# Kernel tuning notes

Hardware: AMD Instinct MI355X
Metric: run time of the kernel (lower is better)

## Reference

```python
import jax, jax.numpy as jnp
import numpy as np

N = 10000; E = 60000; D = 3000; H = 512; L = 128; P = 256
NUM_MASK = 3000  # int(0.3 * N)

def prelu(x, a):
    return jnp.where(x >= 0, x, a * x)

def setup_inputs() -> dict:
    key = jax.random.key(0)
    ks = jax.random.split(key, 32)
    def rn(k, shape, scale=0.02):
        return jax.random.normal(k, shape, jnp.float32) * scale
    inp = {
        'x': jax.random.normal(ks[0], (N, D), jnp.float32),
        'edge_index': jax.random.randint(ks[1], (2, E), 0, N),
        'perm': jax.random.permutation(ks[2], N),
        'shuffle': jax.random.permutation(ks[3], N - NUM_MASK),
        's_W1': rn(ks[4], (D, H)), 's_b1': jnp.zeros((H,), jnp.float32), 's_a': jnp.full((1,), 0.25, jnp.float32),
        's_W2': rn(ks[5], (H, L)), 's_b2': jnp.zeros((L,), jnp.float32),
        't_W1': rn(ks[6], (D, H)), 't_b1': jnp.zeros((H,), jnp.float32), 't_a': jnp.full((1,), 0.25, jnp.float32),
        't_W2': rn(ks[7], (H, L)), 't_b2': jnp.zeros((L,), jnp.float32),
        'p_W1': rn(ks[8], (L, P)), 'p_b1': jnp.zeros((P,), jnp.float32), 'p_a': jnp.full((1,), 0.25, jnp.float32),
        'p_W2': rn(ks[9], (P, L)), 'p_b2': jnp.zeros((L,), jnp.float32),
        'tp_W1': rn(ks[10], (L, P)), 'tp_b1': jnp.zeros((P,), jnp.float32), 'tp_a': jnp.full((1,), 0.25, jnp.float32),
        'tp_W2': rn(ks[11], (P, L)), 'tp_b2': jnp.zeros((L,), jnp.float32),
        'dgi_W': rn(ks[12], (L, L), 0.05),
        'pos_token': rn(ks[13], (1, D)), 'neg_token': rn(ks[14], (1, D)),
        'e2d_W': rn(ks[15], (L, L), 0.05),
        'd_W': rn(ks[16], (L, D)), 'd_b': jnp.zeros((D,), jnp.float32),
    }
    return inp

def reference(x, edge_index, perm, shuffle, s_W1, s_b1, s_a, s_W2, s_b2, t_W1, t_b1, t_a, t_W2, t_b2, p_W1, p_b1, p_a, p_W2, p_b2, tp_W1, tp_b1, tp_a, tp_W2, tp_b2, dgi_W, pos_token, neg_token, e2d_W, d_W, d_b):
    n = x.shape[0]
    # GCN normalization with added self loops (PyG gcn_norm, flow source->target)
    loops = jnp.arange(n)
    src = jnp.concatenate([edge_index[0], loops])
    dst = jnp.concatenate([edge_index[1], loops])
    deg = jax.ops.segment_sum(jnp.ones(dst.shape, x.dtype), dst, n)
    dinv = jnp.where(deg > 0, jax.lax.rsqrt(deg), 0.0)
    enorm = (dinv[src] * dinv[dst])[:, None]  # [E+N, 1]

    def gcn(h, W, b):
        h = h @ W  # transform first, then propagate (PyG GCNConv)
        return jax.ops.segment_sum(h[src] * enorm, dst, n) + b

    # feature masking / corruption (bn=False -> Identity; no dropout at eval)
    mask_nodes = perm[:NUM_MASK]
    keep_nodes = perm[NUM_MASK:]
    use_pos = x.at[mask_nodes].add(pos_token[0])
    use_neg = jnp.zeros_like(x).at[keep_nodes].set(x[keep_nodes][shuffle]).at[mask_nodes].add(neg_token[0])

    # student / teacher two-layer GCN encoders (shared PReLU param per encoder)
    rep_pos = prelu(gcn(prelu(gcn(use_pos, s_W1, s_b1), s_a), s_W2, s_b2), s_a)
    rep_neg = prelu(gcn(prelu(gcn(use_neg, t_W1, t_b1), t_a), t_W2, t_b2), t_a)

    def proj(z, W1, b1, a, W2, b2):
        return prelu(z @ W1 + b1, a) @ W2 + b2

    pos_z = proj(rep_pos[mask_nodes], p_W1, p_b1, p_a, p_W2, p_b2)
    neg_z = proj(rep_neg[mask_nodes], tp_W1, tp_b1, tp_a, tp_W2, tp_b2)

    # DGI loss with sigmoid summary of positive embeddings
    s = jax.nn.sigmoid(pos_z.mean(axis=0))  # [L]
    ws = dgi_W @ s
    pos_d = jax.nn.sigmoid(pos_z @ ws)
    neg_d = jax.nn.sigmoid(neg_z @ ws)
    dgi_loss = -jnp.log(pos_d + 1e-15).mean() - jnp.log(1.0 - neg_d + 1e-15).mean()

    # reconstruction: re-mask latent, single-GCN feature decoder (no activation)
    rec = (rep_pos @ e2d_W).at[mask_nodes].set(0.0)
    rec = gcn(rec, d_W, d_b)

    # SCE loss with alpha = 2
    def l2n(v):
        return v / jnp.maximum(jnp.linalg.norm(v, axis=-1, keepdims=True), 1e-12)
    cos = (l2n(x[mask_nodes]) * l2n(rec[mask_nodes])).sum(axis=-1)
    feat_loss = ((1.0 - cos) ** 2).mean()
    return (feat_loss, dgi_loss)
```

## Files before the change

kernel.cpp:

```cpp
#include <hip/hip_runtime.h>

#define NND 10000
#define EE  60000
#define DD  3000
#define HH  512
#define LL  128
#define PP  256
#define NM  3000

#define KP  3072
#define MP  10240
#define NW  1024
#define KTILES (KP/64)

#define BMT 320
#define BNT 128
#define AH_STR 10240
#define AB_STR 20480
#define BH_STR 4096
#define BB_STR 8192

typedef short bf16x8 __attribute__((ext_vector_type(8)));
typedef float f32x4 __attribute__((ext_vector_type(4)));

__device__ __align__(256) char g_ws[(size_t)176 << 20];

__device__ __forceinline__ unsigned short f2b(float f){
    unsigned int x = __float_as_uint(f);
    unsigned int r = x + 0x7FFFu + ((x >> 16) & 1u);
    return (unsigned short)(r >> 16);
}
__device__ __forceinline__ float b2f(unsigned short u){
    return __uint_as_float(((unsigned int)u) << 16);
}
__device__ __forceinline__ float2 bpair(unsigned int u){
    float2 r;
    r.x = __uint_as_float(u << 16);
    r.y = __uint_as_float(u & 0xffff0000u);
    return r;
}
__device__ __forceinline__ unsigned int packb(float a, float b){
    return (unsigned int)f2b(a) | ((unsigned int)f2b(b) << 16);
}

__device__ __forceinline__ void gl_lds16(const void* g, void* l){
    __builtin_amdgcn_global_load_lds(
        (const __attribute__((address_space(1))) unsigned int*)g,
        (__attribute__((address_space(3))) unsigned int*)l, 16, 0, 0);
}


__global__ void init_k(int* degi, int* cursor, float* scal,
                       float* ptW, float* ntW, float* svecraw, int* ecnt){
    int i = blockIdx.x*256 + threadIdx.x;
    if (i < NND){ degi[i]=0; cursor[i]=0; }
    if (i < 80) scal[i]=0.f;
    if (i == 0) ecnt[0]=0;
    if (i < 128) svecraw[i]=0.f;
    if (i < HH){ ptW[i]=0.f; ntW[i]=0.f; }
}

__global__ void build_k(const int* __restrict__ ei,
                        const int* __restrict__ perm, const int* __restrict__ shuf,
                        int* degi, int* flag, int* negsrc){
    int i = blockIdx.x*256 + threadIdx.x;
    if (i < EE) atomicAdd(&degi[ei[EE + i]], 1);
    if (i < NND){
        int p = perm[i];
        if (i < NM){ flag[p] = 1; negsrc[p] = -1; }
        else       { flag[p] = 0; negsrc[p] = perm[NM + shuf[i - NM]]; }
    }
}

__global__ __launch_bounds__(256) void alloc_k(const int* __restrict__ degi,
                                               float* dinv, int* rowptr, int* ecnt){
    __shared__ int sb[256];
    __shared__ int bbase;
    int t = threadIdx.x;
    int i = blockIdx.x*256 + t;
    int v = (i < NND) ? degi[i] : 0;
    sb[t] = v;
    __syncthreads();
    for (int off = 1; off < 256; off <<= 1){
        int x = 0;
        if (t >= off) x = sb[t - off];
        __syncthreads();
        sb[t] += x;
        __syncthreads();
    }
    if (t == 255) bbase = atomicAdd(ecnt, sb[255]);
    __syncthreads();
    if (i < NND){
        rowptr[i] = bbase + sb[t] - v;
        dinv[i] = 1.f/sqrtf((float)(degi[i] + 1));
    }
}

__global__ void fill_k(const int* __restrict__ ei, const int* __restrict__ rowptr,
                       int* cursor, int* adj){
    int i = blockIdx.x*256 + threadIdx.x;
    if (i < EE){
        int d = ei[EE + i];
        int s = ei[i];
        int p = atomicAdd(&cursor[d], 1);
        adj[rowptr[d] + p] = s;
    }
}

__global__ __launch_bounds__(512) void tok_k(const float* __restrict__ posT,
        const float* __restrict__ negT,
        const float* __restrict__ sW1, const float* __restrict__ tW1,
        float* ptW, float* ntW){
    int b = blockIdx.x; int chunk = blockIdx.y; int j = threadIdx.x;
    const float* tok = b ? negT : posT;
    const float* Wm  = b ? tW1  : sW1;
    float acc = 0.f;
    int d0 = chunk * 47, d1 = d0 + 47; if (d1 > DD) d1 = DD;
    for (int d = d0; d < d1; ++d) acc += tok[d] * Wm[(long)d*HH + j];
    atomicAdd(&((b ? ntW : ptW)[j]), acc);
}


__global__ __launch_bounds__(256) void cast_pad_x_k(const float* __restrict__ x,
                                                    unsigned short* __restrict__ xb){
    long idx = (long)blockIdx.x*256 + threadIdx.x;
    if (idx >= (long)MP*(KP/8)) return;
    int row = (int)(idx / (KP/8));
    int g   = (int)(idx % (KP/8));
    unsigned short o[8] = {0,0,0,0,0,0,0,0};
    if (row < NND && g < DD/8){
        const float* src = x + (long)row*DD + g*8;
        float4 a = *(const float4*)(src);
        float4 b = *(const float4*)(src + 4);
        o[0]=f2b(a.x); o[1]=f2b(a.y); o[2]=f2b(a.z); o[3]=f2b(a.w);
        o[4]=f2b(b.x); o[5]=f2b(b.y); o[6]=f2b(b.z); o[7]=f2b(b.w);
    }
    *(uint4*)(xb + (long)row*KP + g*8) = *(const uint4*)o;
}

struct TBatch {
    const float* in[10];
    unsigned short* out[10];
    int R[10], C[10], OS[10];
    int t0[11];
};

__global__ void transbatch_k(TBatch tb){
    __shared__ unsigned short tile[32][33];
    int b = blockIdx.x;
    int d = 0;
    while (d < 9 && b >= tb.t0[d+1]) d++;
    const float* in = tb.in[d];
    unsigned short* out = tb.out[d];
    int R = tb.R[d], C = tb.C[d], OS = tb.OS[d];
    int lt = b - tb.t0[d];
    int Ctiles = (C + 31) >> 5;
    int rt = lt / Ctiles, ct = lt % Ctiles;
    int rb = rt*32, cb = ct*32;
    int tx = threadIdx.x, ty = threadIdx.y;
    for (int i = ty; i < 32; i += 8){
        int r = rb + i, c = cb + tx;
        tile[i][tx] = (r < R && c < C) ? f2b(in[(long)r*C + c]) : (unsigned short)0;
    }
    __syncthreads();
    for (int i = ty; i < 32; i += 8){
        int c = cb + i, r = rb + tx;
        if (c < C && r < OS) out[(long)c*OS + r] = (r < R) ? tile[tx][i] : (unsigned short)0;
    }
}


#define LDA(PB, MT, KS) (*(const bf16x8*)&As[(PB) + (KS)*AH_STR + a_off + (MT)*512])
#define LDB(PB, NT, KS) (*(const bf16x8*)&Bs[(PB) + (KS)*BH_STR + b_off + (NT)*512])

#define STG_A(KT, PDST, P) gl_lds16(asrc[P] + ((KT)<<6), &As[(PDST) + adst[P]])
#define STG_B(KT, PDST, Q) gl_lds16(bsrc[Q] + ((KT)<<6), &Bs[(PDST) + bdst[Q]])

#define GATE7 asm volatile("s_waitcnt vmcnt(7)" ::: "memory")
#define GATE0 asm volatile("s_waitcnt vmcnt(0)" ::: "memory")
#define NOOPS ((void)0)
#define AFENCE asm volatile("" ::: "memory")
#define BARR  { AFENCE; __builtin_amdgcn_s_barrier(); AFENCE; }

#define TILE_BODY(S1_STMT, S2_STMT, GATE_STMT) {                                  \
    bf16x8 af_[5][2], bf_[4][2];                                                  \
    _Pragma("unroll") for (int nt = 0; nt < 4; ++nt){                             \
        bf_[nt][0] = LDB(pB, nt, 0); bf_[nt][1] = LDB(pB, nt, 1); }               \
    _Pragma("unroll") for (int mt = 0; mt < 5; ++mt){                             \
        af_[mt][0] = LDA(pA, mt, 0); af_[mt][1] = LDA(pA, mt, 1); }               \
    S1_STMT;                                                                      \
    __builtin_amdgcn_s_setprio(1);                                                \
    _Pragma("unroll") for (int ks = 0; ks < 2; ++ks)                              \
      _Pragma("unroll") for (int nt = 0; nt < 4; ++nt)                            \
        _Pragma("unroll") for (int mt = 0; mt < 2; ++mt)                          \
          acc[mt][nt] = __builtin_amdgcn_mfma_f32_16x16x32_bf16(af_[mt][ks], bf_[nt][ks], acc[mt][nt], 0,0,0); \
    __builtin_amdgcn_s_setprio(0);                                                \
    BARR;                                                                         \
    S2_STMT;                                                                      \
    __builtin_amdgcn_s_setprio(1);                                                \
    _Pragma("unroll") for (int ks = 0; ks < 2; ++ks)                              \
      _Pragma("unroll") for (int nt = 0; nt < 4; ++nt)                            \
        _Pragma("unroll") for (int mt = 2; mt < 5; ++mt)                          \
          acc[mt][nt] = __builtin_amdgcn_mfma_f32_16x16x32_bf16(af_[mt][ks], bf_[nt][ks], acc[mt][nt], 0,0,0); \
    __builtin_amdgcn_s_setprio(0);                                                \
    GATE_STMT;                                                                    \
    BARR;                                                                         \
}

__global__ __launch_bounds__(512, 2) void gemm320(
    const unsigned short* __restrict__ Ag,
    const unsigned short* __restrict__ Bg,
    unsigned short* __restrict__ C,
    int M, int Cstride)
{
    __shared__ __align__(1024) unsigned short As[3*AB_STR];
    __shared__ __align__(1024) unsigned short Bs[2*BB_STR];

    const int bid = blockIdx.x;
    const int swz = (bid & 7)*32 + (bid >> 3);
    const int m0 = (swz >> 3) * BMT;
    const int n0 = (swz & 7) * BNT;

    const int tid = threadIdx.x;
    const int w   = tid >> 6,  l = tid & 63;
    const int wm  = w >> 1,    wn = w & 1;
    const int l16 = l & 15,    quad = l >> 4;

    const int schunk = (l & 3) ^ (((l >> 5) & 1) << 1);
    const int rq8   = ((quad ^ (((l16 >> 3) & 1) << 1)) << 3);
    const int a_off = ((wm*80 + l16) << 5) + rq8;
    const int b_off = ((wn*64 + l16) << 5) + rq8;

    const unsigned short* asrc[5]; int adst[5];
    #pragma unroll
    for (int p = 0; p < 5; ++p){
        int j = 5*w + p, kh = j/20, g = j - kh*20;
        asrc[p] = Ag + (long)(m0 + g*16 + (l >> 2))*KP + (kh << 5) + (schunk << 3);
        adst[p] = kh*AH_STR + g*512;
    }
    const unsigned short* bsrc[2]; int bdst[2];
    #pragma unroll
    for (int q = 0; q < 2; ++q){
        int j = 2*w + q, kh = j >> 3, g = j & 7;
        bsrc[q] = Bg + (long)(n0 + g*16 + (l >> 2))*KP + (kh << 5) + (schunk << 3);
        bdst[q] = kh*BH_STR + g*512;
    }

    f32x4 acc[5][4];
    #pragma unroll
    for (int i = 0; i < 5; ++i)
        #pragma unroll
        for (int j = 0; j < 4; ++j)
            #pragma unroll
            for (int r = 0; r < 4; ++r) acc[i][j][r] = 0.f;

    #pragma unroll
    for (int p = 0; p < 5; ++p) STG_A(0, 0, p);
    #pragma unroll
    for (int q = 0; q < 2; ++q) STG_B(0, 0, q);
    #pragma unroll
    for (int p = 0; p < 5; ++p) STG_A(1, AB_STR, p);
    #pragma unroll
    for (int q = 0; q < 2; ++q) STG_B(1, BB_STR, q);
    GATE7;
    BARR;

    int ab = 0, bb = 0;
    #pragma unroll 1
    for (int t = 0; t < KTILES-2; ++t){
        const int pA  = ab*AB_STR;
        const int pB  = bb*BB_STR;
        const int ab2 = (ab == 0) ? 2 : ab - 1;
        const int pA2 = ab2*AB_STR;
        TILE_BODY({ STG_A(t+2,pA2,0); STG_A(t+2,pA2,1); STG_A(t+2,pA2,2); STG_A(t+2,pA2,3); },
                  { STG_A(t+2,pA2,4); STG_B(t+2,pB,0); STG_B(t+2,pB,1); },
                  GATE7)
        ab = (ab == 2) ? 0 : ab + 1;
        bb ^= 1;
    }
    {
        const int pA = ab*AB_STR, pB = bb*BB_STR;
        TILE_BODY(NOOPS, NOOPS, GATE0)
        ab = (ab == 2) ? 0 : ab + 1;
        bb ^= 1;
    }
    {
        const int pA = ab*AB_STR, pB = bb*BB_STR;
        TILE_BODY(NOOPS, NOOPS, NOOPS)
    }

    #pragma unroll
    for (int mt = 0; mt < 5; ++mt){
        const int rowb = m0 + wm*80 + mt*16 + quad*4;
        #pragma unroll
        for (int nt = 0; nt < 4; ++nt){
            const int col = n0 + wn*64 + nt*16 + l16;
            #pragma unroll
            for (int r = 0; r < 4; ++r){
                const int row = rowb + r;
                if (row < M) C[(long)row*Cstride + col] = f2b(acc[mt][nt][r]);
            }
        }
    }
}

__device__ __forceinline__ void gemm_bt_body(
    const unsigned short* __restrict__ A,
    const unsigned short* __restrict__ BT,
    void* __restrict__ Cv,
    int M, int Nn, int K, int Cstride,
    const float* __restrict__ bias,
    const float* __restrict__ alpha,
    int epi, const int* __restrict__ ridx, int obf)
{
    __shared__ __align__(16) unsigned short As[64*40];
    __shared__ __align__(16) unsigned short Bs[64*40];
    const int m0 = blockIdx.y*64, n0 = blockIdx.x*64;
    const int t = threadIdx.x;
    const int lrow = t >> 2, lk = (t & 3) * 8;
    const int wave = t >> 6, lane = t & 63;
    const int quad = lane >> 4, l16 = lane & 15;
    f32x4 acc[4];
    #pragma unroll
    for (int i = 0; i < 4; i++)
        for (int j = 0; j < 4; j++) acc[i][j] = 0.f;

    const bool arv = (m0 + lrow) < M;
    const bool brv = (n0 + lrow) < Nn;
    long arow = 0;
    if (arv) arow = ridx ? (long)ridx[m0 + lrow] : (long)(m0 + lrow);
    const long arowbase = arow * K;
    const long browbase = (long)(n0 + lrow) * K;

    for (int k0 = 0; k0 < K; k0 += 32){
        int gk = k0 + lk;
        uint4 av = {0u,0u,0u,0u};
        uint4 bv = {0u,0u,0u,0u};
        if (arv) av = *(const uint4*)(A + arowbase + gk);
        if (brv) bv = *(const uint4*)(BT + browbase + gk);
        *(uint4*)(&As[lrow*40 + lk]) = av;
        *(uint4*)(&Bs[lrow*40 + lk]) = bv;
        __syncthreads();
        bf16x8 af = *(const bf16x8*)(&As[(wave*16 + l16)*40 + quad*8]);
        #pragma unroll
        for (int nt = 0; nt < 4; nt++){
            bf16x8 bfr = *(const bf16x8*)(&Bs[(nt*16 + l16)*40 + quad*8]);
            acc[nt] = __builtin_amdgcn_mfma_f32_16x16x32_bf16(af, bfr, acc[nt], 0, 0, 0);
        }
        __syncthreads();
    }

    const int rowb = m0 + wave*16 + quad*4;
    float aval = (epi == 2) ? alpha[0] : 0.f;
    #pragma unroll
    for (int nt = 0; nt < 4; nt++){
        int col = n0 + nt*16 + l16;
        if (col >= Nn) continue;
        float bvv = epi ? bias[col] : 0.f;
        #pragma unroll
        for (int r = 0; r < 4; r++){
            int row = rowb + r;
            if (row < M){
                float v = acc[nt][r] + bvv;
                if (epi == 2 && v < 0.f) v *= aval;
                if (obf) ((unsigned short*)Cv)[(long)row*Cstride + col] = f2b(v);
                else     ((float*)Cv)[(long)row*Cstride + col] = v;
            }
        }
    }
}

__global__ __launch_bounds__(256) void gemm_bt_ex(
    const unsigned short* __restrict__ A,
    const unsigned short* __restrict__ BT,
    void* __restrict__ Cv,
    int M, int Nn, int K, int Cstride,
    const float* __restrict__ bias,
    const float* __restrict__ alpha,
    int epi, const int* __restrict__ ridx, int obf)
{
    gemm_bt_body(A, BT, Cv, M, Nn, K, Cstride, bias, alpha, epi, ridx, obf);
}

__global__ __launch_bounds__(256) void gemm_bt2(
    const unsigned short* __restrict__ A0, const unsigned short* __restrict__ A1,
    const unsigned short* __restrict__ B0, const unsigned short* __restrict__ B1,
    void* __restrict__ C0, void* __restrict__ C1,
    int M, int Nn, int K, int Cstride,
    const float* __restrict__ bias0, const float* __restrict__ bias1,
    const float* __restrict__ al0, const float* __restrict__ al1,
    int epi, const int* __restrict__ ridx, int obf)
{
    if (blockIdx.z == 0)
        gemm_bt_body(A0, B0, C0, M, Nn, K, Cstride, bias0, al0, epi, ridx, obf);
    else
        gemm_bt_body(A1, B1, C1, M, Nn, K, Cstride, bias1, al1, epi, ridx, obf);
}

__global__ __launch_bounds__(256) void gemm_bt3(
    const unsigned short* __restrict__ repP, const unsigned short* __restrict__ repN,
    const unsigned short* __restrict__ pW1T, const unsigned short* __restrict__ tpW1T,
    const unsigned short* __restrict__ e2dWT,
    unsigned short* __restrict__ posH, unsigned short* __restrict__ negH,
    unsigned short* __restrict__ recPre,
    const float* __restrict__ pb1, const float* __restrict__ tpb1,
    const float* __restrict__ pa, const float* __restrict__ tpa,
    const int* __restrict__ perm)
{
    int z = blockIdx.z;
    if (z == 0){
        if (blockIdx.y < 47)
            gemm_bt_body(repP, pW1T, posH, NM, PP, LL, PP, pb1, pa, 2, perm, 1);
    } else if (z == 1){
        if (blockIdx.y < 47)
            gemm_bt_body(repN, tpW1T, negH, NM, PP, LL, PP, tpb1, tpa, 2, perm, 1);
    } else {
        if (blockIdx.x < 2)
            gemm_bt_body(repP, e2dWT, recPre, NND, LL, LL, LL, nullptr, nullptr, 0, nullptr, 1);
    }
}


__global__ __launch_bounds__(256) void agg1_k(const unsigned short* __restrict__ XW,
    const float* __restrict__ ptW, const float* __restrict__ ntW,
    const int* __restrict__ flag, const int* __restrict__ negsrc,
    const float* __restrict__ dinv, const int* __restrict__ rowptr,
    const int* __restrict__ degi, const int* __restrict__ adj,
    const float* __restrict__ sb1, const float* __restrict__ sav,
    const float* __restrict__ tb1, const float* __restrict__ tav,
    unsigned short* __restrict__ H1p, unsigned short* __restrict__ H1n)
{
    int i = blockIdx.x; int t = threadIdx.x;
    int c = 2*t;
    float di = dinv[i];
    int rs = rowptr[i], re = rs + degi[i];
    float p0 = ptW[c], p1 = ptW[c+1];
    float n0v = ntW[c], n1v = ntW[c+1];
    int fi = flag[i];
    int nsi = negsrc[i]; if (nsi < 0) nsi = 0;
    float ffi = fi ? 1.f : 0.f;
    float2 xp = bpair(*(const unsigned int*)(XW + (long)i*1024 + c));
    float2 xn = bpair(*(const unsigned int*)(XW + (long)nsi*1024 + 512 + c));
    float pa0 = (xp.x + ffi*p0) * di;
    float pa1 = (xp.y + ffi*p1) * di;
    float na0 = (fi ? n0v : xn.x) * di;
    float na1 = (fi ? n1v : xn.y) * di;
    for (int e = rs; e < re; ++e){
        int s = adj[e]; float ds = dinv[s];
        int fs = flag[s];
        int ns = negsrc[s]; if (ns < 0) ns = 0;
        float ffs = fs ? 1.f : 0.f;
        float2 sp = bpair(*(const unsigned int*)(XW + (long)s*1024 + c));
        float2 sn = bpair(*(const unsigned int*)(XW + (long)ns*1024 + 512 + c));
        pa0 += (sp.x + ffs*p0) * ds;
        pa1 += (sp.y + ffs*p1) * ds;
        na0 += (fs ? n0v : sn.x) * ds;
        na1 += (fs ? n1v : sn.y) * ds;
    }
    float sa_ = sav[0], ta_ = tav[0];
    float v0 = di*pa0 + sb1[c];   if (v0 < 0.f) v0 *= sa_;
    float v1 = di*pa1 + sb1[c+1]; if (v1 < 0.f) v1 *= sa_;
    float w0 = di*na0 + tb1[c];   if (w0 < 0.f) w0 *= ta_;
    float w1 = di*na1 + tb1[c+1]; if (w1 < 0.f) w1 *= ta_;
    *(unsigned int*)(H1p + (long)i*512 + c) = packb(v0, v1);
    *(unsigned int*)(H1n + (long)i*512 + c) = packb(w0, w1);
}

__global__ __launch_bounds__(128) void agg128_k(
    const unsigned short* __restrict__ In0, const unsigned short* __restrict__ In1,
    const float* __restrict__ dinv, const int* __restrict__ rowptr,
    const int* __restrict__ degi, const int* __restrict__ adj,
    const float* __restrict__ b20, const float* __restrict__ b21,
    const float* __restrict__ a20, const float* __restrict__ a21,
    unsigned short* __restrict__ Out0, unsigned short* __restrict__ Out1)
{
    int i = blockIdx.x, t = threadIdx.x;
    int h = blockIdx.y;
    const unsigned short* In = h ? In1 : In0;
    const float* b2 = h ? b21 : b20;
    const float* a2 = h ? a21 : a20;
    unsigned short* Out = h ? Out1 : Out0;
    float di = dinv[i];
    int rs = rowptr[i], re = rs + degi[i];
    float acc = b2f(In[(long)i*128 + t]) * di;
    for (int e = rs; e < re; ++e){
        int s = adj[e];
        acc += b2f(In[(long)s*128 + t]) * dinv[s];
    }
    float v = di*acc + b2[t];
    float a = a2[0]; if (v < 0.f) v *= a;
    Out[(long)i*128 + t] = f2b(v);
}

__global__ __launch_bounds__(128) void aggrec_k(const unsigned short* __restrict__ recPre,
    const float* __restrict__ dinv, const int* __restrict__ rowptr,
    const int* __restrict__ degi, const int* __restrict__ adj,
    const int* __restrict__ flag, const int* __restrict__ perm,
    unsigned short* __restrict__ recAgg)
{
    int b = blockIdx.x, t = threadIdx.x;
    int i = perm[b];
    float di = dinv[i];
    int rs = rowptr[i], re = rs + degi[i];
    float acc = 0.f;
    for (int e = rs; e < re; ++e){
        int s = adj[e];
        if (!flag[s]) acc += b2f(recPre[(long)s*128 + t]) * dinv[s];
    }
    recAgg[(long)b*128 + t] = f2b(di * acc);
}


__global__ __launch_bounds__(128) void meanp_k(const float* __restrict__ posZ,
                                               float* svecraw){
    int j = threadIdx.x;
    int r0 = blockIdx.x*64, r1 = r0 + 64; if (r1 > NM) r1 = NM;
    float s = 0.f;
    for (int r = r0; r < r1; ++r) s += posZ[(long)r*128 + j];
    atomicAdd(&svecraw[j], s);
}

__global__ void ws_k(const float* __restrict__ dgiW, const float* __restrict__ svecraw,
                     float* wsv){
    __shared__ float s[128];
    int i = threadIdx.x;
    s[i] = 1.f/(1.f + expf(-svecraw[i]/(float)NM));
    __syncthreads();
    float a = 0.f;
    for (int j = 0; j < 128; ++j) a += dgiW[i*128 + j] * s[j];
    wsv[i] = a;
}

__global__ __launch_bounds__(256) void dgi_k(const float* __restrict__ posZ,
    const float* __restrict__ negZ, const float* __restrict__ wsv, float* scal){
    __shared__ float sp[4], sn[4];
    int wid = threadIdx.x >> 6, lane = threadIdx.x & 63;
    float w0 = wsv[lane], w1 = wsv[64 + lane];
    float accp = 0.f, accn = 0.f;
    for (int row = blockIdx.x*4 + wid; row < 2*NM; row += gridDim.x*4){
        const float* Z = (row < NM) ? posZ : negZ;
        int r = (row < NM) ? row : row - NM;
        float v = Z[(long)r*128 + lane] * w0 + Z[(long)r*128 + 64 + lane] * w1;
        for (int off = 32; off; off >>= 1) v += __shfl_down(v, off, 64);
        if (lane == 0){
            float d = 1.f/(1.f + expf(-v));
            if (row < NM) accp += logf(d + 1e-15f);
            else          accn += logf(1.f - d + 1e-15f);
        }
    }
    if (lane == 0){ sp[wid] = accp; sn[wid] = accn; }
    __syncthreads();
    if (threadIdx.x == 0){
        atomicAdd(&scal[0], sp[0]+sp[1]+sp[2]+sp[3]);
        atomicAdd(&scal[1], sn[0]+sn[1]+sn[2]+sn[3]);
    }
}


__global__ __launch_bounds__(256) void cos_k(const float* __restrict__ x,
    const unsigned short* __restrict__ recMask, const int* __restrict__ perm,
    float* scal){
    int b = blockIdx.x, t = threadIdx.x;
    long xi = (long)perm[b]*DD;
    long ri = (long)b*DD;
    float dot = 0.f, nx = 0.f, nr = 0.f;
    for (int d = t; d < DD; d += 256){
        float xv = x[xi + d], rv = b2f(recMask[ri + d]);
        dot += xv*rv; nx += xv*xv; nr += rv*rv;
    }
    for (int off = 32; off; off >>= 1){
        dot += __shfl_down(dot, off, 64);
        nx  += __shfl_down(nx,  off, 64);
        nr  += __shfl_down(nr,  off, 64);
    }
    __shared__ float sd[4], sx[4], sr[4];
    int w = t >> 6, lane = t & 63;
    if (lane == 0){ sd[w] = dot; sx[w] = nx; sr[w] = nr; }
    __syncthreads();
    if (t == 0){
        float Dv = sd[0]+sd[1]+sd[2]+sd[3];
        float Xv = sx[0]+sx[1]+sx[2]+sx[3];
        float Rv = sr[0]+sr[1]+sr[2]+sr[3];
        float c = Dv/(fmaxf(sqrtf(Xv),1e-12f)*fmaxf(sqrtf(Rv),1e-12f));
        float e = 1.f - c;
        atomicAdd(&scal[16 + (b & 63)], e*e);
    }
}

__global__ void fin_k(const float* __restrict__ scal, float* out){
    float fs = 0.f;
    for (int i = 0; i < 64; ++i) fs += scal[16 + i];
    float feat = fs/(float)NM;
    float dgi  = -(scal[0]/(float)NM) - (scal[1]/(float)NM);
    out[0] = feat;
    out[1] = dgi;
}


extern "C" void kernel_launch(void* const* d_in, const int* in_sizes, int n_in,
                              void* d_out, int out_size, void* d_ws, size_t ws_size,
                              hipStream_t stream) {
    (void)in_sizes; (void)n_in; (void)out_size; (void)d_ws; (void)ws_size;
    const float* x  = (const float*)d_in[0];
    const int* ei   = (const int*)d_in[1];
    const int* perm = (const int*)d_in[2];
    const int* shuf = (const int*)d_in[3];
    const float* sW1 = (const float*)d_in[4];
    const float* sb1 = (const float*)d_in[5];
    const float* sa  = (const float*)d_in[6];
    const float* sW2 = (const float*)d_in[7];
    const float* sb2 = (const float*)d_in[8];
    const float* tW1 = (const float*)d_in[9];
    const float* tb1 = (const float*)d_in[10];
    const float* ta  = (const float*)d_in[11];
    const float* tW2 = (const float*)d_in[12];
    const float* tb2 = (const float*)d_in[13];
    const float* pW1 = (const float*)d_in[14];
    const float* pb1 = (const float*)d_in[15];
    const float* pa  = (const float*)d_in[16];
    const float* pW2 = (const float*)d_in[17];
    const float* pb2 = (const float*)d_in[18];
    const float* tpW1 = (const float*)d_in[19];
    const float* tpb1 = (const float*)d_in[20];
    const float* tpa  = (const float*)d_in[21];
    const float* tpW2 = (const float*)d_in[22];
    const float* tpb2 = (const float*)d_in[23];
    const float* dgiW = (const float*)d_in[24];
    const float* posT = (const float*)d_in[25];
    const float* negT = (const float*)d_in[26];
    const float* e2dW = (const float*)d_in[27];
    const float* dW   = (const float*)d_in[28];
    const float* db   = (const float*)d_in[29];
    float* out = (float*)d_out;

    void* wsp = nullptr;
    hipGetSymbolAddress(&wsp, HIP_SYMBOL(g_ws));
    char* base = (char*)wsp;
    size_t off = 0;
    auto alloc = [&](size_t b){ size_t o = off; off = (off + b + 255) & ~(size_t)255; return o; };

    float* dinv    = (float*)(base + alloc(NND*4));
    int* degi      = (int*)  (base + alloc(NND*4));
    int* rowptr    = (int*)  (base + alloc(NND*4));
    int* cursor    = (int*)  (base + alloc(NND*4));
    int* adj       = (int*)  (base + alloc(EE*4));
    int* flag      = (int*)  (base + alloc(NND*4));
    int* negsrc    = (int*)  (base + alloc(NND*4));
    int* ecnt      = (int*)  (base + alloc(16*4));
    float* ptW     = (float*)(base + alloc(HH*4));
    float* ntW     = (float*)(base + alloc(HH*4));
    float* svecraw = (float*)(base + alloc(128*4));
    float* wsv     = (float*)(base + alloc(128*4));
    float* scal    = (float*)(base + alloc(80*4));

    unsigned short* xb    = (unsigned short*)(base + alloc((size_t)MP*KP*2));
    unsigned short* W1T   = (unsigned short*)(base + alloc((size_t)NW*KP*2));
    unsigned short* sW2T  = (unsigned short*)(base + alloc((size_t)LL*HH*2));
    unsigned short* tW2T  = (unsigned short*)(base + alloc((size_t)LL*HH*2));
    unsigned short* pW1T  = (unsigned short*)(base + alloc((size_t)PP*LL*2));
    unsigned short* pW2T  = (unsigned short*)(base + alloc((size_t)LL*PP*2));
    unsigned short* tpW1T = (unsigned short*)(base + alloc((size_t)PP*LL*2));
    unsigned short* tpW2T = (unsigned short*)(base + alloc((size_t)LL*PP*2));
    unsigned short* e2dWT = (unsigned short*)(base + alloc((size_t)LL*LL*2));
    unsigned short* dWT   = (unsigned short*)(base + alloc((size_t)DD*LL*2));

    unsigned short* XW      = (unsigned short*)(base + alloc((size_t)NND*1024*2));
    unsigned short* H1p     = (unsigned short*)(base + alloc((size_t)NND*512*2));
    unsigned short* H1n     = (unsigned short*)(base + alloc((size_t)NND*512*2));
    unsigned short* M2p     = (unsigned short*)(base + alloc((size_t)NND*128*2));
    unsigned short* M2n     = (unsigned short*)(base + alloc((size_t)NND*128*2));
    unsigned short* repP    = (unsigned short*)(base + alloc((size_t)NND*128*2));
    unsigned short* repN    = (unsigned short*)(base + alloc((size_t)NND*128*2));
    unsigned short* posH    = (unsigned short*)(base + alloc((size_t)NM*256*2));
    unsigned short* negH    = (unsigned short*)(base + alloc((size_t)NM*256*2));
    float* posZ             = (float*)(base + alloc((size_t)NM*128*4));
    float* negZ             = (float*)(base + alloc((size_t)NM*128*4));
    unsigned short* recPre  = (unsigned short*)(base + alloc((size_t)NND*128*2));
    unsigned short* recAgg  = (unsigned short*)(base + alloc((size_t)NM*128*2));
    unsigned short* recMask = (unsigned short*)(base + alloc((size_t)NM*DD*2));

    init_k<<<(NND+255)/256, 256, 0, stream>>>(degi, cursor, scal, ptW, ntW, svecraw, ecnt);
    build_k<<<(EE+255)/256, 256, 0, stream>>>(ei, perm, shuf, degi, flag, negsrc);
    alloc_k<<<(NND+255)/256, 256, 0, stream>>>(degi, dinv, rowptr, ecnt);
    fill_k<<<(EE+255)/256, 256, 0, stream>>>(ei, rowptr, cursor, adj);
    tok_k<<<dim3(2,64), 512, 0, stream>>>(posT, negT, sW1, tW1, ptW, ntW);

    cast_pad_x_k<<<(int)(((long)MP*(KP/8) + 255)/256), 256, 0, stream>>>(x, xb);
    {
        TBatch tb;
        const float* ins[10] = {sW1, tW1, sW2, tW2, pW1, pW2, tpW1, tpW2, e2dW, dW};
        unsigned short* outs[10] = {W1T, W1T + (size_t)HH*KP, sW2T, tW2T, pW1T, pW2T,
                                    tpW1T, tpW2T, e2dWT, dWT};
        int Rs[10]  = {DD, DD, HH, HH, LL, PP, LL, PP, LL, LL};
        int Cs[10]  = {HH, HH, LL, LL, PP, LL, PP, LL, LL, DD};
        int OSs[10] = {KP, KP, HH, HH, LL, PP, LL, PP, LL, LL};
        int cum = 0;
        for (int d = 0; d < 10; d++){
            tb.in[d] = ins[d]; tb.out[d] = outs[d];
            tb.R[d] = Rs[d]; tb.C[d] = Cs[d]; tb.OS[d] = OSs[d];
            tb.t0[d] = cum;
            cum += (OSs[d]/32) * ((Cs[d] + 31)/32);
        }
        tb.t0[10] = cum;
        transbatch_k<<<cum, dim3(32,8), 0, stream>>>(tb);
    }

    gemm320<<<256, 512, 0, stream>>>(xb, W1T, XW, NND, 1024);
    agg1_k<<<NND, 256, 0, stream>>>(XW, ptW, ntW, flag, negsrc, dinv, rowptr, degi, adj,
                                    sb1, sa, tb1, ta, H1p, H1n);

    gemm_bt2<<<dim3(2,157,2), 256, 0, stream>>>(H1p, H1n, sW2T, tW2T, M2p, M2n,
                                                NND, LL, HH, LL,
                                                nullptr, nullptr, nullptr, nullptr,
                                                0, nullptr, 1);
    agg128_k<<<dim3(NND,2), 128, 0, stream>>>(M2p, M2n, dinv, rowptr, degi, adj,
                                              sb2, tb2, sa, ta, repP, repN);

    gemm_bt3<<<dim3(4,157,3), 256, 0, stream>>>(repP, repN, pW1T, tpW1T, e2dWT,
                                                posH, negH, recPre,
                                                pb1, tpb1, pa, tpa, perm);
    gemm_bt2<<<dim3(2,47,2), 256, 0, stream>>>(posH, negH, pW2T, tpW2T, posZ, negZ,
                                               NM, LL, PP, LL,
                                               pb2, tpb2, nullptr, nullptr, 1, nullptr, 0);

    aggrec_k<<<NM, 128, 0, stream>>>(recPre, dinv, rowptr, degi, adj, flag, perm, recAgg);
    gemm_bt_ex<<<dim3(47,47), 256, 0, stream>>>(recAgg, dWT, recMask, NM, DD, LL, DD,
                                                db, nullptr, 1, nullptr, 1);

    meanp_k<<<47, 128, 0, stream>>>(posZ, svecraw);
    ws_k<<<1, 128, 0, stream>>>(dgiW, svecraw, wsv);
    dgi_k<<<128, 256, 0, stream>>>(posZ, negZ, wsv, scal);

    cos_k<<<NM, 256, 0, stream>>>(x, recMask, perm, scal);

    fin_k<<<1, 1, 0, stream>>>(scal, out);
}
```

Baseline: 509.6 us.

## Double-buffer LDS fragment registers to overlap reads with MFMA in gemm320

Restructures the gemm320 main loop so that the LDS-to-register fragment loads for the next K tile are issued while the MFMAs of the current tile run, using two register fragment sets (A/B ping-pong). The loop is unrolled by two, and global-to-LDS staging is interleaved differently with a vmcnt(4) gate. The aim is to hide ds_read latency behind matrix math. The extra fragment registers raise VGPR pressure under launch_bounds(512,2), which could cause spills. The changed barrier and buffer-rotation logic also needs to stay correct for the LDS buffers.

```diff
diff --git a/kernel.cpp b/kernel.cpp
--- a/kernel.cpp
+++ b/kernel.cpp
@@ -176,36 +176,32 @@
 #define STG_A(KT, PDST, P) gl_lds16(asrc[P] + ((KT)<<6), &As[(PDST) + adst[P]])
 #define STG_B(KT, PDST, Q) gl_lds16(bsrc[Q] + ((KT)<<6), &Bs[(PDST) + bdst[Q]])
 
-#define GATE7 asm volatile("s_waitcnt vmcnt(7)" ::: "memory")
+#define GATE4 asm volatile("s_waitcnt vmcnt(4)" ::: "memory")
 #define GATE0 asm volatile("s_waitcnt vmcnt(0)" ::: "memory")
-#define NOOPS ((void)0)
 #define AFENCE asm volatile("" ::: "memory")
 #define BARR  { AFENCE; __builtin_amdgcn_s_barrier(); AFENCE; }
 
-#define TILE_BODY(S1_STMT, S2_STMT, GATE_STMT) {                                  \
-    bf16x8 af_[5][2], bf_[4][2];                                                  \
-    _Pragma("unroll") for (int nt = 0; nt < 4; ++nt){                             \
-        bf_[nt][0] = LDB(pB, nt, 0); bf_[nt][1] = LDB(pB, nt, 1); }               \
-    _Pragma("unroll") for (int mt = 0; mt < 5; ++mt){                             \
-        af_[mt][0] = LDA(pA, mt, 0); af_[mt][1] = LDA(pA, mt, 1); }               \
-    S1_STMT;                                                                      \
+#define CL1(AF, BF)                                                               \
     __builtin_amdgcn_s_setprio(1);                                                \
     _Pragma("unroll") for (int ks = 0; ks < 2; ++ks)                              \
       _Pragma("unroll") for (int nt = 0; nt < 4; ++nt)                            \
         _Pragma("unroll") for (int mt = 0; mt < 2; ++mt)                          \
-          acc[mt][nt] = __builtin_amdgcn_mfma_f32_16x16x32_bf16(af_[mt][ks], bf_[nt][ks], acc[mt][nt], 0,0,0); \
-    __builtin_amdgcn_s_setprio(0);                                                \
-    BARR;                                                                         \
-    S2_STMT;                                                                      \
+          acc[mt][nt] = __builtin_amdgcn_mfma_f32_16x16x32_bf16(AF[mt][ks], BF[nt][ks], acc[mt][nt], 0,0,0); \
+    __builtin_amdgcn_s_setprio(0);
+
+#define CL2(AF, BF)                                                               \
     __builtin_amdgcn_s_setprio(1);                                                \
     _Pragma("unroll") for (int ks = 0; ks < 2; ++ks)                              \
       _Pragma("unroll") for (int nt = 0; nt < 4; ++nt)                            \
         _Pragma("unroll") for (int mt = 2; mt < 5; ++mt)                          \
-          acc[mt][nt] = __builtin_amdgcn_mfma_f32_16x16x32_bf16(af_[mt][ks], bf_[nt][ks], acc[mt][nt], 0,0,0); \
-    __builtin_amdgcn_s_setprio(0);                                                \
-    GATE_STMT;                                                                    \
-    BARR;                                                                         \
-}
+          acc[mt][nt] = __builtin_amdgcn_mfma_f32_16x16x32_bf16(AF[mt][ks], BF[nt][ks], acc[mt][nt], 0,0,0); \
+    __builtin_amdgcn_s_setprio(0);
+
+#define RDF(AF, BF, PA, PB)                                                       \
+    _Pragma("unroll") for (int nt = 0; nt < 4; ++nt){                             \
+        BF[nt][0] = LDB(PB, nt, 0); BF[nt][1] = LDB(PB, nt, 1); }                 \
+    _Pragma("unroll") for (int mt = 0; mt < 5; ++mt){                             \
+        AF[mt][0] = LDA(PA, mt, 0); AF[mt][1] = LDA(PA, mt, 1); }
 
 __global__ __launch_bounds__(512, 2) void gemm320(
     const unsigned short* __restrict__ Ag,
@@ -254,6 +250,8 @@
             #pragma unroll
             for (int r = 0; r < 4; ++r) acc[i][j][r] = 0.f;
 
+    bf16x8 afA[5][2], bfA[4][2], afB[5][2], bfB[4][2];
+
     #pragma unroll
     for (int p = 0; p < 5; ++p) STG_A(0, 0, p);
     #pragma unroll
@@ -262,32 +260,40 @@
     for (int p = 0; p < 5; ++p) STG_A(1, AB_STR, p);
     #pragma unroll
     for (int q = 0; q < 2; ++q) STG_B(1, BB_STR, q);
-    GATE7;
+    asm volatile("s_waitcnt vmcnt(7)" ::: "memory");
     BARR;
-
-    int ab = 0, bb = 0;
+    RDF(afA, bfA, 0, 0);
+
+    int ab = 0;
     #pragma unroll 1
-    for (int t = 0; t < KTILES-2; ++t){
-        const int pA  = ab*AB_STR;
-        const int pB  = bb*BB_STR;
-        const int ab2 = (ab == 0) ? 2 : ab - 1;
-        const int pA2 = ab2*AB_STR;
-        TILE_BODY({ STG_A(t+2,pA2,0); STG_A(t+2,pA2,1); STG_A(t+2,pA2,2); STG_A(t+2,pA2,3); },
-                  { STG_A(t+2,pA2,4); STG_B(t+2,pB,0); STG_B(t+2,pB,1); },
-                  GATE7)
-        ab = (ab == 2) ? 0 : ab + 1;
-        bb ^= 1;
+    for (int p = 0; p < (KTILES-2)/2; ++p){
+        const int t  = 2*p;
+        const int a0 = ab*AB_STR;
+        const int a1 = ((ab == 2) ? 0 : ab + 1)*AB_STR;
+        const int a2 = ((ab == 0) ? 2 : ab - 1)*AB_STR;
+        STG_A(t+2, a2, 0); STG_A(t+2, a2, 1); STG_A(t+2, a2, 2); STG_A(t+2, a2, 3);
+        CL1(afA, bfA);
+        GATE4; BARR;
+        STG_A(t+2, a2, 4); STG_B(t+2, 0, 0); STG_B(t+2, 0, 1);
+        RDF(afB, bfB, a1, BB_STR);
+        CL2(afA, bfA);
+        STG_A(t+3, a0, 0); STG_A(t+3, a0, 1); STG_A(t+3, a0, 2); STG_A(t+3, a0, 3);
+        CL1(afB, bfB);
+        GATE4; BARR;
+        STG_A(t+3, a0, 4); STG_B(t+3, BB_STR, 0); STG_B(t+3, BB_STR, 1);
+        RDF(afA, bfA, a2, 0);
+        CL2(afB, bfB);
+        ab = (ab == 0) ? 2 : ab - 1;
     }
     {
-        const int pA = ab*AB_STR, pB = bb*BB_STR;
-        TILE_BODY(NOOPS, NOOPS, GATE0)
-        ab = (ab == 2) ? 0 : ab + 1;
-        bb ^= 1;
-    }
-    {
-        const int pA = ab*AB_STR, pB = bb*BB_STR;
-        TILE_BODY(NOOPS, NOOPS, NOOPS)
-    }
+        const int a1 = ((ab == 2) ? 0 : ab + 1)*AB_STR;
+        CL1(afA, bfA);
+        GATE0; BARR;
+        RDF(afB, bfB, a1, BB_STR);
+        CL2(afA, bfA);
+    }
+    CL1(afB, bfB);
+    CL2(afB, bfB);
 
     #pragma unroll
     for (int mt = 0; mt < 5; ++mt){
```

Result: slower. 520.7 us (+2.2%).
